# Kernel tuning notes

Measured on AMD Instinct MI355X. Metric: run time of the kernel, lower is better.

## Reference

```python
import jax, jax.numpy as jnp
import numpy as np

B, NSP, H, W = 8, 1024, 256, 256   # frames, superpixels/frame, label-map size
N = B * NSP                        # total superpixel nodes
MIX = 0.5                          # mixing_coeff
SIGMA = 0.05


def _interp_axis(x, out, axis):
    # 1-D bilinear interpolation along `axis`, align_corners=True
    n = x.shape[axis]
    pos = jnp.linspace(0.0, n - 1.0, out).astype(x.dtype)
    i0 = jnp.floor(pos).astype(jnp.int32)
    i1 = jnp.minimum(i0 + 1, n - 1)
    wt = pos - i0.astype(x.dtype)
    shp = [1] * x.ndim
    shp[axis] = out
    wt = wt.reshape(shp)
    return jnp.take(x, i0, axis=axis) * (1 - wt) + jnp.take(x, i1, axis=axis) * wt


def _upsample_ac(x, oh, ow):
    # nn.UpsamplingBilinear2d (align_corners=True)
    if x.shape[2] == oh and x.shape[3] == ow:
        return x
    return _interp_axis(_interp_axis(x, oh, 2), ow, 3)


def _sp_pool(feats, seg):
    # upsample [B,C,h,w] to label resolution, then average features per superpixel -> [N, C]
    C = feats.shape[1]
    up = _upsample_ac(feats, H, W)
    vals = up.transpose(0, 2, 3, 1).reshape(-1, C)          # [B*H*W, C]
    sums = jax.ops.segment_sum(vals, seg, num_segments=N)
    cnt = jax.ops.segment_sum(jnp.ones((seg.shape[0],), vals.dtype), seg, num_segments=N)
    return sums / jnp.maximum(cnt, 1.0)[:, None]


def _gcn(x, Wm, b, src, dst, ew):
    # GCNConv(normalize=False): out_i = sum_{j->i} ew * (x_j @ W) + b
    h = x @ Wm
    agg = jax.ops.segment_sum(h[src] * ew[:, None], dst, num_segments=x.shape[0])
    return agg + b


def _coord_map():
    # channel 0 varies along dim2 (w), channel 1 varies along dim3 (h), both in [0,1]
    c0 = jnp.broadcast_to((jnp.arange(H, dtype=jnp.float32) / (H - 1))[:, None], (H, W))
    c1 = jnp.broadcast_to((jnp.arange(W, dtype=jnp.float32) / (W - 1))[None, :], (H, W))
    return jnp.broadcast_to(jnp.stack([c0, c1], 0)[None], (B, 2, H, W))


def setup_inputs() -> dict:
    key = jax.random.key(0)
    ks = jax.random.split(key, 12)
    labels = jax.random.randint(ks[0], (B, 1, H, W), 0, NSP, dtype=jnp.int32)
    skip0 = jax.random.normal(ks[1], (B, 512, 32, 32), jnp.float32)
    skip1 = jax.random.normal(ks[2], (B, 256, 64, 64), jnp.float32)
    skip2 = jax.random.normal(ks[3], (B, 256, 128, 128), jnp.float32)
    E = 131072
    edges_nn = jax.random.randint(ks[4], (2, E), 0, N, dtype=jnp.int32)
    negs = jax.random.randint(ks[5], (E,), 0, N, dtype=jnp.int32)
    W0 = jax.random.normal(ks[6], (512, 256), jnp.float32) / np.float32(np.sqrt(512))
    W1 = jax.random.normal(ks[7], (256, 256), jnp.float32) / np.float32(np.sqrt(256))
    W2 = jax.random.normal(ks[8], (256, 256), jnp.float32) / np.float32(np.sqrt(256))
    lin_w = jax.random.normal(ks[9], (256, 1), jnp.float32) / np.float32(np.sqrt(256))
    z = jnp.zeros((256,), jnp.float32)
    return {"labels": labels, "skip0": skip0, "skip1": skip1, "skip2": skip2,
            "edges_nn": edges_nn, "negs": negs,
            "W0": W0, "b0": z, "W1": W1, "b1": z, "W2": W2, "b2": z, "lin_w": lin_w}


def reference(labels, skip0, skip1, skip2, edges_nn, negs, W0, b0, W1, b1, W2, b2, lin_w):
    # per-pixel global superpixel id (offset per frame)
    seg = (labels.reshape(B, -1) + NSP * jnp.arange(B, dtype=labels.dtype)[:, None]).reshape(-1)
    src, dst = edges_nn[0], edges_nn[1]

    # pooled normalized coordinates per superpixel -> gaussian edge weights
    pc = _sp_pool(_coord_map(), seg)                        # [N, 2]
    dr = pc[src] - pc[dst]
    dist = jnp.linalg.norm(dr, axis=1)
    edge_attr = jnp.exp(-dist ** 2 / SIGMA)

    x = _sp_pool(skip0, seg)                                # [N, 512]
    layers = [(W0, b0, None), (W1, b1, skip1), (W2, b2, skip2)]
    for i, (Wm, b, sk) in enumerate(layers):
        if i > 0:
            x = (1 - MIX) * x + MIX * _sp_pool(sk, seg)
        x = jax.nn.relu(_gcn(x, Wm, b, src, dst, edge_attr))

    s = x @ lin_w                                           # [N, 1]
    dap = jax.nn.sigmoid(s[src] - s[dst])
    dan = jax.nn.sigmoid(s[src] - s[negs])
    return dan, dap, edge_attr
```

## Files before the change

kernel.cpp:

```cpp
#include <hip/hip_runtime.h>
#include <hip/hip_fp16.h>
#include <cstdint>
#include <cstddef>

#define BB 8
#define NSPX 1024
#define NNODE 8192
#define EE 131072
#define NPIX 524288
#define CH 256

typedef unsigned int uint;
typedef unsigned long long u64;

__device__ __forceinline__ uint packh2(float a, float b) {
  __half2 h = __float22half2_rn(make_float2(a, b));
  return *reinterpret_cast<uint*>(&h);
}
__device__ __forceinline__ __half2 uh2(uint u) { return *reinterpret_cast<__half2*>(&u); }
__device__ __forceinline__ uint h2u(__half2 h) { return *reinterpret_cast<uint*>(&h); }

__global__ __launch_bounds__(256) void zero_kernel(int4* p, int n4) {
  int i = blockIdx.x * 256 + threadIdx.x;
  int stride = gridDim.x * 256;
  int4 z = make_int4(0, 0, 0, 0);
  for (; i < n4; i += stride) p[i] = z;
}

__global__ __launch_bounds__(256) void cnt2_kernel(const int* __restrict__ labels,
                                                   const int* __restrict__ edst,
                                                   int* __restrict__ segb,
                                                   u64* __restrict__ packed,
                                                   int* __restrict__ cnt_e) {
  int blk = blockIdx.x;
  int t = threadIdx.x;
  if (blk < 2048) {
    int p = blk * 256 + t;
    int b = p >> 16;
    int h = (p >> 8) & 255;
    int w = p & 255;
    int seg = labels[p] + (b << 10);
    segb[p] = seg;
    u64 enc = (1ULL << 48) | ((u64)h << 24) | (u64)w;
    atomicAdd(&packed[seg], enc);
  } else {
    int e = (blk - 2048) * 256 + t;
    atomicAdd(&cnt_e[edst[e]], 1);
  }
}

__global__ __launch_bounds__(1024) void scan2_kernel(const u64* __restrict__ packed,
                                                     const int* __restrict__ cnt_e,
                                                     int* __restrict__ poff, int* __restrict__ eoff) {
  __shared__ int ps[1024];
  int which = blockIdx.x;
  int* coff = which ? eoff : poff;
  int t = threadIdx.x;
  int base = t * 8;
  int v[8];
  int sum = 0;
#pragma unroll
  for (int i = 0; i < 8; ++i) {
    int x = which ? cnt_e[base + i] : (int)(packed[base + i] >> 48);
    v[i] = sum;
    sum += x;
  }
  ps[t] = sum;
  __syncthreads();
  for (int off = 1; off < 1024; off <<= 1) {
    int x = (t >= off) ? ps[t - off] : 0;
    __syncthreads();
    ps[t] += x;
    __syncthreads();
  }
  int prev = (t == 0) ? 0 : ps[t - 1];
#pragma unroll
  for (int i = 0; i < 8; ++i) coff[base + i] = prev + v[i];
  if (t == 1023) coff[8192] = ps[1023];
}

__global__ __launch_bounds__(256) void rcnt_kernel(const u64* __restrict__ packed,
                                                   float* __restrict__ rcnt,
                                                   float* __restrict__ pch, float* __restrict__ pcw) {
  int n = blockIdx.x * 256 + threadIdx.x;
  if (n >= NNODE) return;
  u64 v = packed[n];
  int c = (int)(v >> 48);
  int sh = (int)((v >> 24) & 0xFFFFFF);
  int sw = (int)(v & 0xFFFFFF);
  float r = 1.0f / (float)(c > 1 ? c : 1);
  rcnt[n] = r;
  pch[n] = (float)sh * r * (1.0f / 255.0f);
  pcw[n] = (float)sw * r * (1.0f / 255.0f);
}

__global__ __launch_bounds__(256) void scatter2_kernel(const int* __restrict__ segb,
                                                       const int* __restrict__ poff,
                                                       int* __restrict__ pcur,
                                                       int* __restrict__ psorted,
                                                       const int* __restrict__ esrc,
                                                       const int* __restrict__ edst,
                                                       const float* __restrict__ pch,
                                                       const float* __restrict__ pcw,
                                                       const int* __restrict__ eoff,
                                                       int* __restrict__ ecur,
                                                       uint2* __restrict__ evw,
                                                       float* __restrict__ outp) {
  int blk = blockIdx.x;
  int t = threadIdx.x;
  if (blk < 2048) {
    int p = blk * 256 + t;
    int s = segb[p];
    int pos = poff[s] + atomicAdd(&pcur[s], 1);
    psorted[pos] = p;
  } else {
    int e = (blk - 2048) * 256 + t;
    int s1 = esrc[e], d1 = edst[e];
    float dh = pch[s1] - pch[d1];
    float dw = pcw[s1] - pcw[d1];
    float ea = expf(-(dh * dh + dw * dw) * 20.0f);
    outp[2 * EE + e] = ea;
    int pos = eoff[d1] + atomicAdd(&ecur[d1], 1);
    evw[pos] = make_uint2((uint)s1, __float_as_uint(ea));
  }
}

__global__ __launch_bounds__(256) void gemm_kmaj_f16(const float* __restrict__ A,
                                                     const float* __restrict__ W,
                                                     __half* __restrict__ out) {
  __shared__ float As[64][36];
  int b = blockIdx.z;
  int m0 = blockIdx.x * 32;
  int n0 = blockIdx.y * 128;
  int t = threadIdx.x;
  int ct = t & 31;
  int rm = t >> 5;
  int l8 = t & 7, kr = t >> 3;
  const float* Ab = A + (size_t)b * 512 * 1024;
  float4 acc[4];
#pragma unroll
  for (int i = 0; i < 4; ++i) acc[i] = make_float4(0.f, 0.f, 0.f, 0.f);
  for (int k0 = 0; k0 < 512; k0 += 64) {
#pragma unroll
    for (int pass = 0; pass < 2; ++pass) {
      int k = kr + pass * 32;
      float4 v = *(const float4*)&Ab[(size_t)(k0 + k) * 1024 + m0 + l8 * 4];
      *(float4*)&As[k][l8 * 4] = v;
    }
    __syncthreads();
#pragma unroll 8
    for (int k = 0; k < 64; ++k) {
      float4 a = *(const float4*)&As[k][rm * 4];
      float4 wv = *(const float4*)&W[(size_t)(k0 + k) * 256 + n0 + ct * 4];
      acc[0].x += a.x * wv.x; acc[0].y += a.x * wv.y; acc[0].z += a.x * wv.z; acc[0].w += a.x * wv.w;
      acc[1].x += a.y * wv.x; acc[1].y += a.y * wv.y; acc[1].z += a.y * wv.z; acc[1].w += a.y * wv.w;
      acc[2].x += a.z * wv.x; acc[2].y += a.z * wv.y; acc[2].z += a.z * wv.z; acc[2].w += a.z * wv.w;
      acc[3].x += a.w * wv.x; acc[3].y += a.w * wv.y; acc[3].z += a.w * wv.z; acc[3].w += a.w * wv.w;
    }
    __syncthreads();
  }
#pragma unroll
  for (int i = 0; i < 4; ++i) {
    int m = m0 + rm * 4 + i;
    uint2 pk = make_uint2(packh2(acc[i].x, acc[i].y), packh2(acc[i].z, acc[i].w));
    *(uint2*)&out[((size_t)b * 1024 + m) * 256 + n0 + ct * 4] = pk;
  }
}

__global__ __launch_bounds__(256) void transpose64_f16(const float* __restrict__ src, __half* __restrict__ dst,
                                                       int C, int P) {
  __shared__ float tile[64][65];
  int b = blockIdx.z;
  int p0 = blockIdx.x * 64;
  int c0 = blockIdx.y * 64;
  int t = threadIdx.x;
  int l16 = t & 15, r16 = t >> 4;
#pragma unroll
  for (int pass = 0; pass < 4; ++pass) {
    int c = r16 + pass * 16;
    float4 v = *(const float4*)&src[((size_t)b * C + c0 + c) * P + p0 + l16 * 4];
    tile[c][l16 * 4 + 0] = v.x;
    tile[c][l16 * 4 + 1] = v.y;
    tile[c][l16 * 4 + 2] = v.z;
    tile[c][l16 * 4 + 3] = v.w;
  }
  __syncthreads();
  int l8 = t & 7, r32 = t >> 3;
#pragma unroll
  for (int pass = 0; pass < 2; ++pass) {
    int p = r32 + pass * 32;
    uint r[4];
#pragma unroll
    for (int q = 0; q < 4; ++q)
      r[q] = packh2(tile[l8 * 8 + 2 * q][p], tile[l8 * 8 + 2 * q + 1][p]);
    *(uint4*)&dst[((size_t)b * P + p0 + p) * C + c0 + l8 * 8] = make_uint4(r[0], r[1], r[2], r[3]);
  }
}

__device__ __forceinline__ void tap16(const __half* __restrict__ tp, float wt, __half2* acc) {
  uint4 qa = *(const uint4*)tp;
  uint4 qb = *(const uint4*)(tp + 8);
  __half2 W = __float2half2_rn(wt);
  acc[0] = __hfma2(W, uh2(qa.x), acc[0]);
  acc[1] = __hfma2(W, uh2(qa.y), acc[1]);
  acc[2] = __hfma2(W, uh2(qa.z), acc[2]);
  acc[3] = __hfma2(W, uh2(qa.w), acc[3]);
  acc[4] = __hfma2(W, uh2(qb.x), acc[4]);
  acc[5] = __hfma2(W, uh2(qb.y), acc[5]);
  acc[6] = __hfma2(W, uh2(qb.z), acc[6]);
  acc[7] = __hfma2(W, uh2(qb.w), acc[7]);
}

template <int HS>
__device__ __forceinline__ void taps16(const __half* __restrict__ fb, int h, int w, __half2* acc) {
  const float fh = (float)(HS - 1) / 255.0f;
  float ph = h * fh, pw = w * fh;
  int i0 = (int)ph, j0 = (int)pw;
  float th = ph - (float)i0, tw = pw - (float)j0;
  int i1 = min(i0 + 1, HS - 1), jj1 = min(j0 + 1, HS - 1);
  float w11 = th * tw, w10 = th - w11, w01 = tw - w11, w00 = 1.f - th - tw + w11;
  tap16(fb + (i0 * HS + j0) * 256, w00, acc);
  tap16(fb + (i0 * HS + jj1) * 256, w01, acc);
  tap16(fb + (i1 * HS + j0) * 256, w10, acc);
  tap16(fb + (i1 * HS + jj1) * 256, w11, acc);
}

__global__ __launch_bounds__(256) void gather01_kernel(const __half* __restrict__ F0,
                                                       const __half* __restrict__ F1,
                                                       const int* __restrict__ poff,
                                                       const int* __restrict__ psorted,
                                                       const float* __restrict__ rc,
                                                       __half* __restrict__ p0out,
                                                       float* __restrict__ p1out) {
  int blk = blockIdx.x;
  int n = ((blk & 7) << 10) | (blk >> 3);
  int b = n >> 10;
  int t = threadIdx.x;
  int l = t & 15;
  int s = t >> 4;
  const __half* f0 = F0 + (size_t)b * 1024 * 256 + l * 16;
  const __half* f1 = F1 + (size_t)b * 4096 * 256 + l * 16;
  int j1 = poff[n + 1];
  __half2 z = __float2half2_rn(0.f);
  __half2 a0[8], a1[8];
#pragma unroll
  for (int i = 0; i < 8; ++i) { a0[i] = z; a1[i] = z; }
  for (int j = poff[n] + s; j < j1; j += 16) {
    int p = psorted[j];
    int h = (p >> 8) & 255, w = p & 255;
    taps16<32>(f0, h, w, a0);
    taps16<64>(f1, h, w, a1);
  }
  __shared__ uint red[2][256][9];
#pragma unroll
  for (int k = 0; k < 8; ++k) { red[0][t][k] = h2u(a0[k]); red[1][t][k] = h2u(a1[k]); }
  __syncthreads();
  if (t < 128) {
    int l2 = t >> 3, k = t & 7;
    float r = rc[n];
    float2 s0 = make_float2(0.f, 0.f), s1 = s0;
#pragma unroll
    for (int ss = 0; ss < 16; ++ss) {
      float2 v0 = __half22float2(uh2(red[0][ss * 16 + l2][k]));
      float2 v1 = __half22float2(uh2(red[1][ss * 16 + l2][k]));
      s0.x += v0.x; s0.y += v0.y;
      s1.x += v1.x; s1.y += v1.y;
    }
    int c = l2 * 16 + k * 2;
    *(uint*)&p0out[(size_t)n * 256 + c] = packh2(s0.x * r, s0.y * r);
    *(float2*)&p1out[(size_t)n * 256 + c] = make_float2(s1.x * r, s1.y * r);
  }
}

__global__ __launch_bounds__(256) void gather2_kernel(const __half* __restrict__ F,
                                                      const int* __restrict__ poff,
                                                      const int* __restrict__ psorted,
                                                      const float* __restrict__ rc,
                                                      float* __restrict__ pout) {
  int blk = blockIdx.x;
  int n = ((blk & 7) << 10) | (blk >> 3);
  int b = n >> 10;
  int c0 = blockIdx.y * 128;
  int t = threadIdx.x;
  int l = t & 7;
  int s = t >> 3;
  const __half* fb = F + (size_t)b * 16384 * 256 + c0 + l * 16;
  int j1 = poff[n + 1];
  __half2 z = __float2half2_rn(0.f);
  __half2 acc[8];
#pragma unroll
  for (int i = 0; i < 8; ++i) acc[i] = z;
  for (int j = poff[n] + s; j < j1; j += 32) {
    int p = psorted[j];
    int h = (p >> 8) & 255, w = p & 255;
    taps16<128>(fb, h, w, acc);
  }
  __shared__ uint red[256][9];
#pragma unroll
  for (int k = 0; k < 8; ++k) red[t][k] = h2u(acc[k]);
  __syncthreads();
  if (t < 64) {
    int l2 = t >> 3, k = t & 7;
    float r = rc[n];
    float2 sm = make_float2(0.f, 0.f);
#pragma unroll
    for (int ss = 0; ss < 32; ++ss) {
      float2 v = __half22float2(uh2(red[ss * 8 + l2][k]));
      sm.x += v.x; sm.y += v.y;
    }
    int c = c0 + l2 * 16 + k * 2;
    *(float2*)&pout[(size_t)n * 256 + c] = make_float2(sm.x * r, sm.y * r);
  }
}

__global__ __launch_bounds__(256) void gemm_mix_n256(const float* __restrict__ X, const float* __restrict__ Pl,
                                                     const float* __restrict__ W, __half* __restrict__ out) {
  const int t = threadIdx.x;
  const int r0 = blockIdx.x * 16;
  const int cw = (t & 63) * 4;
  const int rg = (t >> 6) * 4;
  __shared__ float Xl[16][68];
  float4 acc[4];
#pragma unroll
  for (int i = 0; i < 4; ++i) acc[i] = make_float4(0.f, 0.f, 0.f, 0.f);
  for (int k0 = 0; k0 < 256; k0 += 64) {
#pragma unroll
    for (int l = 0; l < 4; ++l) {
      int idx = t + 256 * l;
      int r = idx >> 6, k = idx & 63;
      size_t a = (size_t)(r0 + r) * 256 + k0 + k;
      Xl[r][k] = 0.5f * (X[a] + Pl[a]);
    }
    __syncthreads();
#pragma unroll
    for (int k4 = 0; k4 < 64; k4 += 4) {
      float4 a[4];
#pragma unroll
      for (int i = 0; i < 4; ++i) a[i] = *(const float4*)&Xl[rg + i][k4];
#pragma unroll
      for (int kk = 0; kk < 4; ++kk) {
        float4 w = *(const float4*)&W[(size_t)(k0 + k4 + kk) * 256 + cw];
#pragma unroll
        for (int i = 0; i < 4; ++i) {
          float av = ((const float*)&a[i])[kk];
          acc[i].x += av * w.x;
          acc[i].y += av * w.y;
          acc[i].z += av * w.z;
          acc[i].w += av * w.w;
        }
      }
    }
    __syncthreads();
  }
#pragma unroll
  for (int i = 0; i < 4; ++i) {
    uint2 pk = make_uint2(packh2(acc[i].x, acc[i].y), packh2(acc[i].z, acc[i].w));
    *(uint2*)&out[(size_t)(r0 + rg + i) * 256 + cw] = pk;
  }
}

__global__ __launch_bounds__(256) void agg_kernel(const __half* __restrict__ h, const float* __restrict__ bias,
                                                  const int* __restrict__ eoff,
                                                  const uint2* __restrict__ evw,
                                                  float* __restrict__ xout) {
  int n = blockIdx.x * 2 + (threadIdx.x >> 7);
  int c2 = threadIdx.x & 127;
  int e0 = eoff[n], e1 = eoff[n + 1];
  float a0 = 0.f, a1 = 0.f;
  for (int j = e0; j < e1; ++j) {
    uint2 ev = evw[j];
    float wv = __uint_as_float(ev.y);
    uint hv = *(const uint*)&h[((size_t)ev.x << 8) + c2 * 2];
    float2 f = __half22float2(uh2(hv));
    a0 += wv * f.x;
    a1 += wv * f.y;
  }
  float v0 = a0 + bias[2 * c2];
  float v1 = a1 + bias[2 * c2 + 1];
  float2 st = make_float2(v0 > 0.f ? v0 : 0.f, v1 > 0.f ? v1 : 0.f);
  *(float2*)&xout[((size_t)n << 8) + 2 * c2] = st;
}

__global__ __launch_bounds__(256) void score_kernel(const float* __restrict__ x, const float* __restrict__ lw,
                                                    float* __restrict__ s) {
  int t = threadIdx.x;
  int n = blockIdx.x * 4 + (t >> 6);
  int lane = t & 63;
  const float* row = x + ((size_t)n << 8);
  float v = row[lane] * lw[lane] + row[lane + 64] * lw[lane + 64] +
            row[lane + 128] * lw[lane + 128] + row[lane + 192] * lw[lane + 192];
#pragma unroll
  for (int off = 32; off > 0; off >>= 1) v += __shfl_down(v, off, 64);
  if (lane == 0) s[n] = v;
}

__global__ __launch_bounds__(256) void out_kernel(const float* __restrict__ s, const int* __restrict__ src,
                                                  const int* __restrict__ dst, const int* __restrict__ negs,
                                                  float* __restrict__ outp) {
  int e = blockIdx.x * 256 + threadIdx.x;
  if (e >= EE) return;
  float ss = s[src[e]];
  float a = ss - s[negs[e]];
  float b = ss - s[dst[e]];
  outp[e] = 1.0f / (1.0f + expf(-a));
  outp[EE + e] = 1.0f / (1.0f + expf(-b));
}

extern "C" void kernel_launch(void* const* d_in, const int* in_sizes, int n_in,
                              void* d_out, int out_size, void* d_ws, size_t ws_size,
                              hipStream_t stream) {
  const int*   labels = (const int*)d_in[0];
  const float* skip0  = (const float*)d_in[1];
  const float* skip1  = (const float*)d_in[2];
  const float* skip2  = (const float*)d_in[3];
  const int*   edges  = (const int*)d_in[4];
  const int*   negs   = (const int*)d_in[5];
  const float* W0     = (const float*)d_in[6];
  const float* b0     = (const float*)d_in[7];
  const float* W1     = (const float*)d_in[8];
  const float* b1     = (const float*)d_in[9];
  const float* W2     = (const float*)d_in[10];
  const float* b2     = (const float*)d_in[11];
  const float* lw     = (const float*)d_in[12];
  const int* esrc = edges;
  const int* edst = edges + EE;
  float* outp = (float*)d_out;

  size_t o = 0;
  char* base = (char*)d_ws;
  auto alloc = [&](size_t bytes) -> void* {
    void* p = base + o;
    o += (bytes + 255) & ~(size_t)255;
    return p;
  };
  u64* packed  = (u64*)alloc(NNODE * 8);
  int* cnt_e   = (int*)alloc(NNODE * 4);
  int* ecur    = (int*)alloc(NNODE * 4);
  int* pcur    = (int*)alloc(NNODE * 4);
  size_t zbytes = o;
  float*  rcnt    = (float*)alloc(NNODE * 4);
  float*  pch     = (float*)alloc(NNODE * 4);
  float*  pcw     = (float*)alloc(NNODE * 4);
  int*    poff    = (int*)alloc((NNODE + 1) * 4);
  int*    eoff    = (int*)alloc((NNODE + 1) * 4);
  uint2*  evw     = (uint2*)alloc((size_t)EE * 8);
  int*    psorted = (int*)alloc(NPIX * 4);
  int*    segb    = (int*)alloc(NPIX * 4);
  float*  bufA    = (float*)alloc((size_t)NNODE * CH * 4);
  float*  bufB    = (float*)alloc((size_t)NNODE * CH * 4);
  float*  p1buf   = (float*)alloc((size_t)NNODE * CH * 4);
  float*  p2buf   = (float*)alloc((size_t)NNODE * CH * 4);
  __half* h0b     = (__half*)alloc((size_t)NNODE * CH * 2);
  __half* h1b     = (__half*)alloc((size_t)NNODE * CH * 2);
  __half* F0b     = (__half*)alloc((size_t)BB * 1024 * CH * 2);
  __half* F1t     = (__half*)alloc((size_t)BB * 4096 * CH * 2);
  __half* F2t     = (__half*)alloc((size_t)BB * 16384 * CH * 2);
  float*  sbuf    = (float*)alloc(NNODE * 4);
  (void)ws_size; (void)n_in; (void)in_sizes; (void)out_size;

  zero_kernel<<<64, 256, 0, stream>>>((int4*)d_ws, (int)(zbytes / 16));
  cnt2_kernel<<<2048 + 512, 256, 0, stream>>>(labels, edst, segb, packed, cnt_e);
  scan2_kernel<<<2, 1024, 0, stream>>>(packed, cnt_e, poff, eoff);
  rcnt_kernel<<<NNODE / 256, 256, 0, stream>>>(packed, rcnt, pch, pcw);
  scatter2_kernel<<<2048 + 512, 256, 0, stream>>>(segb, poff, pcur, psorted,
                                                  esrc, edst, pch, pcw, eoff, ecur, evw, outp);
  gemm_kmaj_f16<<<dim3(32, 2, BB), 256, 0, stream>>>(skip0, W0, F0b);
  transpose64_f16<<<dim3(4096 / 64, 4, BB), 256, 0, stream>>>(skip1, F1t, 256, 4096);
  transpose64_f16<<<dim3(16384 / 64, 4, BB), 256, 0, stream>>>(skip2, F2t, 256, 16384);
  gather01_kernel<<<NNODE, 256, 0, stream>>>(F0b, F1t, poff, psorted, rcnt, h0b, p1buf);
  gather2_kernel<<<dim3(NNODE, 2), 256, 0, stream>>>(F2t, poff, psorted, rcnt, p2buf);
  agg_kernel<<<NNODE / 2, 256, 0, stream>>>(h0b, b0, eoff, evw, bufB);
  gemm_mix_n256<<<NNODE / 16, 256, 0, stream>>>(bufB, p1buf, W1, h1b);
  agg_kernel<<<NNODE / 2, 256, 0, stream>>>(h1b, b1, eoff, evw, bufA);
  gemm_mix_n256<<<NNODE / 16, 256, 0, stream>>>(bufA, p2buf, W2, h1b);
  agg_kernel<<<NNODE / 2, 256, 0, stream>>>(h1b, b2, eoff, evw, bufB);
  score_kernel<<<NNODE / 4, 256, 0, stream>>>(bufB, lw, sbuf);
  out_kernel<<<EE / 256, 256, 0, stream>>>(sbuf, esrc, edst, negs, outp);
}
```

Baseline: 726.1 us.

## Merge independent preprocessing kernels into horizontally fused launches

Combines the counting pass, the skip1/skip2 transposes and the skip0 GEMM into one interleaved launch. It also merges the scan with the reciprocal-count kernel, and the two gather kernels into one grid. The aim is to cut launch overhead and the idle tails between small dependent kernels, so that compute- and bandwidth-bound work can overlap on the GPU. The cost is larger shared memory per block for every branch and divergent block roles, which may lower occupancy for the lighter work.

```diff
diff --git a/kernel.cpp b/kernel.cpp
--- a/kernel.cpp
+++ b/kernel.cpp
@@ -27,71 +27,164 @@
   for (; i < n4; i += stride) p[i] = z;
 }
 
-__global__ __launch_bounds__(256) void cnt2_kernel(const int* __restrict__ labels,
-                                                   const int* __restrict__ edst,
-                                                   int* __restrict__ segb,
-                                                   u64* __restrict__ packed,
-                                                   int* __restrict__ cnt_e) {
+__device__ __forceinline__ void dev_transpose(const float* __restrict__ src, __half* __restrict__ dst,
+                                              int C, int P, int b, int p0, int c0, int t,
+                                              float (*tile)[65]) {
+  int l16 = t & 15, r16 = t >> 4;
+#pragma unroll
+  for (int pass = 0; pass < 4; ++pass) {
+    int c = r16 + pass * 16;
+    float4 v = *(const float4*)&src[((size_t)b * C + c0 + c) * P + p0 + l16 * 4];
+    tile[c][l16 * 4 + 0] = v.x;
+    tile[c][l16 * 4 + 1] = v.y;
+    tile[c][l16 * 4 + 2] = v.z;
+    tile[c][l16 * 4 + 3] = v.w;
+  }
+  __syncthreads();
+  int l8 = t & 7, r32 = t >> 3;
+#pragma unroll
+  for (int pass = 0; pass < 2; ++pass) {
+    int p = r32 + pass * 32;
+    uint r[4];
+#pragma unroll
+    for (int q = 0; q < 4; ++q)
+      r[q] = packh2(tile[l8 * 8 + 2 * q][p], tile[l8 * 8 + 2 * q + 1][p]);
+    *(uint4*)&dst[((size_t)b * P + p0 + p) * C + c0 + l8 * 8] = make_uint4(r[0], r[1], r[2], r[3]);
+  }
+}
+
+__device__ __forceinline__ void dev_gemm_kmaj(const float* __restrict__ A, const float* __restrict__ W,
+                                              __half* __restrict__ out, int idx, int t,
+                                              float (*As)[36]) {
+  int b = idx >> 6;
+  int m0 = (idx & 31) * 32;
+  int n0 = ((idx >> 5) & 1) * 128;
+  int ct = t & 31;
+  int rm = t >> 5;
+  int l8 = t & 7, kr = t >> 3;
+  const float* Ab = A + (size_t)b * 512 * 1024;
+  float4 acc[4];
+#pragma unroll
+  for (int i = 0; i < 4; ++i) acc[i] = make_float4(0.f, 0.f, 0.f, 0.f);
+  for (int k0 = 0; k0 < 512; k0 += 64) {
+#pragma unroll
+    for (int pass = 0; pass < 2; ++pass) {
+      int k = kr + pass * 32;
+      float4 v = *(const float4*)&Ab[(size_t)(k0 + k) * 1024 + m0 + l8 * 4];
+      *(float4*)&As[k][l8 * 4] = v;
+    }
+    __syncthreads();
+#pragma unroll 8
+    for (int k = 0; k < 64; ++k) {
+      float4 a = *(const float4*)&As[k][rm * 4];
+      float4 wv = *(const float4*)&W[(size_t)(k0 + k) * 256 + n0 + ct * 4];
+      acc[0].x += a.x * wv.x; acc[0].y += a.x * wv.y; acc[0].z += a.x * wv.z; acc[0].w += a.x * wv.w;
+      acc[1].x += a.y * wv.x; acc[1].y += a.y * wv.y; acc[1].z += a.y * wv.z; acc[1].w += a.y * wv.w;
+      acc[2].x += a.z * wv.x; acc[2].y += a.z * wv.y; acc[2].z += a.z * wv.z; acc[2].w += a.z * wv.w;
+      acc[3].x += a.w * wv.x; acc[3].y += a.w * wv.y; acc[3].z += a.w * wv.z; acc[3].w += a.w * wv.w;
+    }
+    __syncthreads();
+  }
+#pragma unroll
+  for (int i = 0; i < 4; ++i) {
+    int m = m0 + rm * 4 + i;
+    uint2 pk = make_uint2(packh2(acc[i].x, acc[i].y), packh2(acc[i].z, acc[i].w));
+    *(uint2*)&out[((size_t)b * 1024 + m) * 256 + n0 + ct * 4] = pk;
+  }
+}
+
+__global__ __launch_bounds__(256) void fusedA_kernel(const int* __restrict__ labels,
+                                                     const int* __restrict__ edst,
+                                                     int* __restrict__ segb,
+                                                     u64* __restrict__ packed,
+                                                     int* __restrict__ cnt_e,
+                                                     const float* __restrict__ skip0,
+                                                     const float* __restrict__ W0,
+                                                     __half* __restrict__ F0b,
+                                                     const float* __restrict__ skip1,
+                                                     __half* __restrict__ F1t,
+                                                     const float* __restrict__ skip2,
+                                                     __half* __restrict__ F2t) {
+  __shared__ __align__(16) char smem[16640];
   int blk = blockIdx.x;
   int t = threadIdx.x;
-  if (blk < 2048) {
-    int p = blk * 256 + t;
-    int b = p >> 16;
-    int h = (p >> 8) & 255;
-    int w = p & 255;
-    int seg = labels[p] + (b << 10);
-    segb[p] = seg;
-    u64 enc = (1ULL << 48) | ((u64)h << 24) | (u64)w;
-    atomicAdd(&packed[seg], enc);
+  int s = blk % 26;
+  int q = blk / 26;
+  if (s < 16) {
+    int idx = q * 16 + s;
+    int p0 = (idx & 255) * 64;
+    int c0 = ((idx >> 8) & 3) * 64;
+    int b = idx >> 10;
+    dev_transpose(skip2, F2t, 256, 16384, b, p0, c0, t, (float(*)[65])smem);
+  } else if (s < 20) {
+    int idx = q * 4 + (s - 16);
+    int p0 = (idx & 63) * 64;
+    int c0 = ((idx >> 6) & 3) * 64;
+    int b = idx >> 8;
+    dev_transpose(skip1, F1t, 256, 4096, b, p0, c0, t, (float(*)[65])smem);
+  } else if (s < 25) {
+    int idx = q * 5 + (s - 20);
+    if (idx < 2048) {
+      int p = idx * 256 + t;
+      int b = p >> 16;
+      int h = (p >> 8) & 255;
+      int w = p & 255;
+      int seg = labels[p] + (b << 10);
+      segb[p] = seg;
+      u64 enc = (1ULL << 48) | ((u64)h << 24) | (u64)w;
+      atomicAdd(&packed[seg], enc);
+    } else {
+      int e = (idx - 2048) * 256 + t;
+      atomicAdd(&cnt_e[edst[e]], 1);
+    }
   } else {
-    int e = (blk - 2048) * 256 + t;
-    atomicAdd(&cnt_e[edst[e]], 1);
-  }
-}
-
-__global__ __launch_bounds__(1024) void scan2_kernel(const u64* __restrict__ packed,
-                                                     const int* __restrict__ cnt_e,
-                                                     int* __restrict__ poff, int* __restrict__ eoff) {
-  __shared__ int ps[1024];
-  int which = blockIdx.x;
-  int* coff = which ? eoff : poff;
+    dev_gemm_kmaj(skip0, W0, F0b, q, t, (float(*)[36])smem);
+  }
+}
+
+__global__ __launch_bounds__(1024) void fusedB_kernel(const u64* __restrict__ packed,
+                                                      const int* __restrict__ cnt_e,
+                                                      int* __restrict__ poff, int* __restrict__ eoff,
+                                                      float* __restrict__ rcnt,
+                                                      float* __restrict__ pch, float* __restrict__ pcw) {
+  int blk = blockIdx.x;
   int t = threadIdx.x;
-  int base = t * 8;
-  int v[8];
-  int sum = 0;
-#pragma unroll
-  for (int i = 0; i < 8; ++i) {
-    int x = which ? cnt_e[base + i] : (int)(packed[base + i] >> 48);
-    v[i] = sum;
-    sum += x;
-  }
-  ps[t] = sum;
-  __syncthreads();
-  for (int off = 1; off < 1024; off <<= 1) {
-    int x = (t >= off) ? ps[t - off] : 0;
-    __syncthreads();
-    ps[t] += x;
-    __syncthreads();
-  }
-  int prev = (t == 0) ? 0 : ps[t - 1];
-#pragma unroll
-  for (int i = 0; i < 8; ++i) coff[base + i] = prev + v[i];
-  if (t == 1023) coff[8192] = ps[1023];
-}
-
-__global__ __launch_bounds__(256) void rcnt_kernel(const u64* __restrict__ packed,
-                                                   float* __restrict__ rcnt,
-                                                   float* __restrict__ pch, float* __restrict__ pcw) {
-  int n = blockIdx.x * 256 + threadIdx.x;
-  if (n >= NNODE) return;
-  u64 v = packed[n];
-  int c = (int)(v >> 48);
-  int sh = (int)((v >> 24) & 0xFFFFFF);
-  int sw = (int)(v & 0xFFFFFF);
-  float r = 1.0f / (float)(c > 1 ? c : 1);
-  rcnt[n] = r;
-  pch[n] = (float)sh * r * (1.0f / 255.0f);
-  pcw[n] = (float)sw * r * (1.0f / 255.0f);
+  if (blk < 2) {
+    __shared__ int ps[1024];
+    int which = blk;
+    int* coff = which ? eoff : poff;
+    int base = t * 8;
+    int v[8];
+    int sum = 0;
+#pragma unroll
+    for (int i = 0; i < 8; ++i) {
+      int x = which ? cnt_e[base + i] : (int)(packed[base + i] >> 48);
+      v[i] = sum;
+      sum += x;
+    }
+    ps[t] = sum;
+    __syncthreads();
+    for (int off = 1; off < 1024; off <<= 1) {
+      int x = (t >= off) ? ps[t - off] : 0;
+      __syncthreads();
+      ps[t] += x;
+      __syncthreads();
+    }
+    int prev = (t == 0) ? 0 : ps[t - 1];
+#pragma unroll
+    for (int i = 0; i < 8; ++i) coff[base + i] = prev + v[i];
+    if (t == 1023) coff[8192] = ps[1023];
+  } else {
+    int n = (blk - 2) * 1024 + t;
+    u64 v = packed[n];
+    int c = (int)(v >> 48);
+    int sh = (int)((v >> 24) & 0xFFFFFF);
+    int sw = (int)(v & 0xFFFFFF);
+    float r = 1.0f / (float)(c > 1 ? c : 1);
+    rcnt[n] = r;
+    pch[n] = (float)sh * r * (1.0f / 255.0f);
+    pcw[n] = (float)sw * r * (1.0f / 255.0f);
+  }
 }
 
 __global__ __launch_bounds__(256) void scatter2_kernel(const int* __restrict__ segb,
@@ -125,78 +218,6 @@
   }
 }
 
-__global__ __launch_bounds__(256) void gemm_kmaj_f16(const float* __restrict__ A,
-                                                     const float* __restrict__ W,
-                                                     __half* __restrict__ out) {
-  __shared__ float As[64][36];
-  int b = blockIdx.z;
-  int m0 = blockIdx.x * 32;
-  int n0 = blockIdx.y * 128;
-  int t = threadIdx.x;
-  int ct = t & 31;
-  int rm = t >> 5;
-  int l8 = t & 7, kr = t >> 3;
-  const float* Ab = A + (size_t)b * 512 * 1024;
-  float4 acc[4];
-#pragma unroll
-  for (int i = 0; i < 4; ++i) acc[i] = make_float4(0.f, 0.f, 0.f, 0.f);
-  for (int k0 = 0; k0 < 512; k0 += 64) {
-#pragma unroll
-    for (int pass = 0; pass < 2; ++pass) {
-      int k = kr + pass * 32;
-      float4 v = *(const float4*)&Ab[(size_t)(k0 + k) * 1024 + m0 + l8 * 4];
-      *(float4*)&As[k][l8 * 4] = v;
-    }
-    __syncthreads();
-#pragma unroll 8
-    for (int k = 0; k < 64; ++k) {
-      float4 a = *(const float4*)&As[k][rm * 4];
-      float4 wv = *(const float4*)&W[(size_t)(k0 + k) * 256 + n0 + ct * 4];
-      acc[0].x += a.x * wv.x; acc[0].y += a.x * wv.y; acc[0].z += a.x * wv.z; acc[0].w += a.x * wv.w;
-      acc[1].x += a.y * wv.x; acc[1].y += a.y * wv.y; acc[1].z += a.y * wv.z; acc[1].w += a.y * wv.w;
-      acc[2].x += a.z * wv.x; acc[2].y += a.z * wv.y; acc[2].z += a.z * wv.z; acc[2].w += a.z * wv.w;
-      acc[3].x += a.w * wv.x; acc[3].y += a.w * wv.y; acc[3].z += a.w * wv.z; acc[3].w += a.w * wv.w;
-    }
-    __syncthreads();
-  }
-#pragma unroll
-  for (int i = 0; i < 4; ++i) {
-    int m = m0 + rm * 4 + i;
-    uint2 pk = make_uint2(packh2(acc[i].x, acc[i].y), packh2(acc[i].z, acc[i].w));
-    *(uint2*)&out[((size_t)b * 1024 + m) * 256 + n0 + ct * 4] = pk;
-  }
-}
-
-__global__ __launch_bounds__(256) void transpose64_f16(const float* __restrict__ src, __half* __restrict__ dst,
-                                                       int C, int P) {
-  __shared__ float tile[64][65];
-  int b = blockIdx.z;
-  int p0 = blockIdx.x * 64;
-  int c0 = blockIdx.y * 64;
-  int t = threadIdx.x;
-  int l16 = t & 15, r16 = t >> 4;
-#pragma unroll
-  for (int pass = 0; pass < 4; ++pass) {
-    int c = r16 + pass * 16;
-    float4 v = *(const float4*)&src[((size_t)b * C + c0 + c) * P + p0 + l16 * 4];
-    tile[c][l16 * 4 + 0] = v.x;
-    tile[c][l16 * 4 + 1] = v.y;
-    tile[c][l16 * 4 + 2] = v.z;
-    tile[c][l16 * 4 + 3] = v.w;
-  }
-  __syncthreads();
-  int l8 = t & 7, r32 = t >> 3;
-#pragma unroll
-  for (int pass = 0; pass < 2; ++pass) {
-    int p = r32 + pass * 32;
-    uint r[4];
-#pragma unroll
-    for (int q = 0; q < 4; ++q)
-      r[q] = packh2(tile[l8 * 8 + 2 * q][p], tile[l8 * 8 + 2 * q + 1][p]);
-    *(uint4*)&dst[((size_t)b * P + p0 + p) * C + c0 + l8 * 8] = make_uint4(r[0], r[1], r[2], r[3]);
-  }
-}
-
 __device__ __forceinline__ void tap16(const __half* __restrict__ tp, float wt, __half2* acc) {
   uint4 qa = *(const uint4*)tp;
   uint4 qb = *(const uint4*)(tp + 8);
@@ -225,91 +246,91 @@
   tap16(fb + (i1 * HS + jj1) * 256, w11, acc);
 }
 
-__global__ __launch_bounds__(256) void gather01_kernel(const __half* __restrict__ F0,
-                                                       const __half* __restrict__ F1,
-                                                       const int* __restrict__ poff,
-                                                       const int* __restrict__ psorted,
-                                                       const float* __restrict__ rc,
-                                                       __half* __restrict__ p0out,
-                                                       float* __restrict__ p1out) {
+__global__ __launch_bounds__(256) void fusedC_kernel(const __half* __restrict__ F0,
+                                                     const __half* __restrict__ F1,
+                                                     const __half* __restrict__ F2,
+                                                     const int* __restrict__ poff,
+                                                     const int* __restrict__ psorted,
+                                                     const float* __restrict__ rc,
+                                                     __half* __restrict__ p0out,
+                                                     float* __restrict__ p1out,
+                                                     float* __restrict__ p2out) {
+  __shared__ __align__(16) char smem[18432];
   int blk = blockIdx.x;
-  int n = ((blk & 7) << 10) | (blk >> 3);
-  int b = n >> 10;
   int t = threadIdx.x;
-  int l = t & 15;
-  int s = t >> 4;
-  const __half* f0 = F0 + (size_t)b * 1024 * 256 + l * 16;
-  const __half* f1 = F1 + (size_t)b * 4096 * 256 + l * 16;
-  int j1 = poff[n + 1];
-  __half2 z = __float2half2_rn(0.f);
-  __half2 a0[8], a1[8];
-#pragma unroll
-  for (int i = 0; i < 8; ++i) { a0[i] = z; a1[i] = z; }
-  for (int j = poff[n] + s; j < j1; j += 16) {
-    int p = psorted[j];
-    int h = (p >> 8) & 255, w = p & 255;
-    taps16<32>(f0, h, w, a0);
-    taps16<64>(f1, h, w, a1);
-  }
-  __shared__ uint red[2][256][9];
-#pragma unroll
-  for (int k = 0; k < 8; ++k) { red[0][t][k] = h2u(a0[k]); red[1][t][k] = h2u(a1[k]); }
-  __syncthreads();
-  if (t < 128) {
-    int l2 = t >> 3, k = t & 7;
-    float r = rc[n];
-    float2 s0 = make_float2(0.f, 0.f), s1 = s0;
-#pragma unroll
-    for (int ss = 0; ss < 16; ++ss) {
-      float2 v0 = __half22float2(uh2(red[0][ss * 16 + l2][k]));
-      float2 v1 = __half22float2(uh2(red[1][ss * 16 + l2][k]));
-      s0.x += v0.x; s0.y += v0.y;
-      s1.x += v1.x; s1.y += v1.y;
-    }
-    int c = l2 * 16 + k * 2;
-    *(uint*)&p0out[(size_t)n * 256 + c] = packh2(s0.x * r, s0.y * r);
-    *(float2*)&p1out[(size_t)n * 256 + c] = make_float2(s1.x * r, s1.y * r);
-  }
-}
-
-__global__ __launch_bounds__(256) void gather2_kernel(const __half* __restrict__ F,
-                                                      const int* __restrict__ poff,
-                                                      const int* __restrict__ psorted,
-                                                      const float* __restrict__ rc,
-                                                      float* __restrict__ pout) {
-  int blk = blockIdx.x;
-  int n = ((blk & 7) << 10) | (blk >> 3);
-  int b = n >> 10;
-  int c0 = blockIdx.y * 128;
-  int t = threadIdx.x;
-  int l = t & 7;
-  int s = t >> 3;
-  const __half* fb = F + (size_t)b * 16384 * 256 + c0 + l * 16;
-  int j1 = poff[n + 1];
-  __half2 z = __float2half2_rn(0.f);
-  __half2 acc[8];
-#pragma unroll
-  for (int i = 0; i < 8; ++i) acc[i] = z;
-  for (int j = poff[n] + s; j < j1; j += 32) {
-    int p = psorted[j];
-    int h = (p >> 8) & 255, w = p & 255;
-    taps16<128>(fb, h, w, acc);
-  }
-  __shared__ uint red[256][9];
-#pragma unroll
-  for (int k = 0; k < 8; ++k) red[t][k] = h2u(acc[k]);
-  __syncthreads();
-  if (t < 64) {
-    int l2 = t >> 3, k = t & 7;
-    float r = rc[n];
-    float2 sm = make_float2(0.f, 0.f);
-#pragma unroll
-    for (int ss = 0; ss < 32; ++ss) {
-      float2 v = __half22float2(uh2(red[ss * 8 + l2][k]));
-      sm.x += v.x; sm.y += v.y;
-    }
-    int c = c0 + l2 * 16 + k * 2;
-    *(float2*)&pout[(size_t)n * 256 + c] = make_float2(sm.x * r, sm.y * r);
+  if (blk >= 8192 && blk < 16384) {
+    int x = blk - 8192;
+    int n = ((x & 7) << 10) | (x >> 3);
+    int b = n >> 10;
+    int l = t & 15;
+    int s = t >> 4;
+    const __half* f0 = F0 + (size_t)b * 1024 * 256 + l * 16;
+    const __half* f1 = F1 + (size_t)b * 4096 * 256 + l * 16;
+    int j1 = poff[n + 1];
+    __half2 z = __float2half2_rn(0.f);
+    __half2 a0[8], a1[8];
+#pragma unroll
+    for (int i = 0; i < 8; ++i) { a0[i] = z; a1[i] = z; }
+    for (int j = poff[n] + s; j < j1; j += 16) {
+      int p = psorted[j];
+      int h = (p >> 8) & 255, w = p & 255;
+      taps16<32>(f0, h, w, a0);
+      taps16<64>(f1, h, w, a1);
+    }
+    uint (*red)[256][9] = (uint(*)[256][9])smem;
+#pragma unroll
+    for (int k = 0; k < 8; ++k) { red[0][t][k] = h2u(a0[k]); red[1][t][k] = h2u(a1[k]); }
+    __syncthreads();
+    if (t < 128) {
+      int l2 = t >> 3, k = t & 7;
+      float r = rc[n];
+      float2 s0 = make_float2(0.f, 0.f), s1 = s0;
+#pragma unroll
+      for (int ss = 0; ss < 16; ++ss) {
+        float2 v0 = __half22float2(uh2(red[0][ss * 16 + l2][k]));
+        float2 v1 = __half22float2(uh2(red[1][ss * 16 + l2][k]));
+        s0.x += v0.x; s0.y += v0.y;
+        s1.x += v1.x; s1.y += v1.y;
+      }
+      int c = l2 * 16 + k * 2;
+      *(uint*)&p0out[(size_t)n * 256 + c] = packh2(s0.x * r, s0.y * r);
+      *(float2*)&p1out[(size_t)n * 256 + c] = make_float2(s1.x * r, s1.y * r);
+    }
+  } else {
+    int x, c0;
+    if (blk < 8192) { x = blk; c0 = 0; }
+    else            { x = blk - 16384; c0 = 128; }
+    int n = ((x & 7) << 10) | (x >> 3);
+    int b = n >> 10;
+    int l = t & 7;
+    int s = t >> 3;
+    const __half* fb = F2 + (size_t)b * 16384 * 256 + c0 + l * 16;
+    int j1 = poff[n + 1];
+    __half2 z = __float2half2_rn(0.f);
+    __half2 acc[8];
+#pragma unroll
+    for (int i = 0; i < 8; ++i) acc[i] = z;
+    for (int j = poff[n] + s; j < j1; j += 32) {
+      int p = psorted[j];
+      int h = (p >> 8) & 255, w = p & 255;
+      taps16<128>(fb, h, w, acc);
+    }
+    uint (*red)[9] = (uint(*)[9])smem;
+#pragma unroll
+    for (int k = 0; k < 8; ++k) red[t][k] = h2u(acc[k]);
+    __syncthreads();
+    if (t < 64) {
+      int l2 = t >> 3, k = t & 7;
+      float r = rc[n];
+      float2 sm = make_float2(0.f, 0.f);
+#pragma unroll
+      for (int ss = 0; ss < 32; ++ss) {
+        float2 v = __half22float2(uh2(red[ss * 8 + l2][k]));
+        sm.x += v.x; sm.y += v.y;
+      }
+      int c = c0 + l2 * 16 + k * 2;
+      *(float2*)&p2out[(size_t)n * 256 + c] = make_float2(sm.x * r, sm.y * r);
+    }
   }
 }
 
@@ -459,16 +480,13 @@
   (void)ws_size; (void)n_in; (void)in_sizes; (void)out_size;
 
   zero_kernel<<<64, 256, 0, stream>>>((int4*)d_ws, (int)(zbytes / 16));
-  cnt2_kernel<<<2048 + 512, 256, 0, stream>>>(labels, edst, segb, packed, cnt_e);
-  scan2_kernel<<<2, 1024, 0, stream>>>(packed, cnt_e, poff, eoff);
-  rcnt_kernel<<<NNODE / 256, 256, 0, stream>>>(packed, rcnt, pch, pcw);
+  fusedA_kernel<<<13312, 256, 0, stream>>>(labels, edst, segb, packed, cnt_e,
+                                           skip0, W0, F0b, skip1, F1t, skip2, F2t);
+  fusedB_kernel<<<10, 1024, 0, stream>>>(packed, cnt_e, poff, eoff, rcnt, pch, pcw);
   scatter2_kernel<<<2048 + 512, 256, 0, stream>>>(segb, poff, pcur, psorted,
                                                   esrc, edst, pch, pcw, eoff, ecur, evw, outp);
-  gemm_kmaj_f16<<<dim3(32, 2, BB), 256, 0, stream>>>(skip0, W0, F0b);
-  transpose64_f16<<<dim3(4096 / 64, 4, BB), 256, 0, stream>>>(skip1, F1t, 256, 4096);
-  transpose64_f16<<<dim3(16384 / 64, 4, BB), 256, 0, stream>>>(skip2, F2t, 256, 16384);
-  gather01_kernel<<<NNODE, 256, 0, stream>>>(F0b, F1t, poff, psorted, rcnt, h0b, p1buf);
-  gather2_kernel<<<dim3(NNODE, 2), 256, 0, stream>>>(F2t, poff, psorted, rcnt, p2buf);
+  fusedC_kernel<<<24576, 256, 0, stream>>>(F0b, F1t, F2t, poff, psorted, rcnt,
+                                           h0b, p1buf, p2buf);
   agg_kernel<<<NNODE / 2, 256, 0, stream>>>(h0b, b0, eoff, evw, bufB);
   gemm_mix_n256<<<NNODE / 16, 256, 0, stream>>>(bufB, p1buf, W1, h1b);
   agg_kernel<<<NNODE / 2, 256, 0, stream>>>(h1b, b1, eoff, evw, bufA);
```

New measurement: 719.4 us. About the same (-0.9%).
